# Kernel tuning notes

Hardware: AMD Instinct MI355X
Metric: run time of the kernel (lower is better)

Reference implementation:

```python
import math
import jax, jax.numpy as jnp
import numpy as np

HIDDEN = 1024
N_HEADS = 16
HEAD = HIDDEN // N_HEADS
B = 2
L = 2048
STRIDE = 128
EXPR = 8
MAXPOS = 2048


def _checkpoint(wi):
    if wi % STRIDE == 0 and wi != 0:
        return wi - EXPR
    return (wi // STRIDE) * STRIDE + STRIDE - EXPR


def _subset_summaries(absolute_max):
    ci = _checkpoint(0)
    s = set()
    while ci <= absolute_max - 1:
        s |= set(range(ci, min(ci + EXPR + 1, absolute_max)))
        ci = _checkpoint(ci + STRIDE)
    return s


def build_sparse_mask(n, bidirectional=True):
    # Faithful numpy port of prepare_sparse_mask: -1e4 everywhere, 0 at allowed positions.
    mask = np.full((n, n), -10000.0, dtype=np.float32)
    global_summaries = _subset_summaries(n) if bidirectional else set()
    for i in range(n):
        absolute_max = n if bidirectional else i + 1
        rounded = ((i + STRIDE) // STRIDE) * STRIDE
        if i % STRIDE == 0 and i != 0:
            s1 = set(range(i - STRIDE, min(absolute_max, i + 1)))
        else:
            s1 = set(range(max(0, rounded - STRIDE), min(absolute_max, rounded + 1)))
        s2 = set() if bidirectional else _subset_summaries(absolute_max)
        idx = sorted(s1 | s2 | global_summaries)
        mask[i, idx] = 0.0
    return mask


def setup_inputs() -> dict:
    key = jax.random.key(0)
    ks = jax.random.split(key, 8)
    s = 1.0 / math.sqrt(HIDDEN)
    inp = {
        "hidden_states": jax.random.normal(ks[0], (B, L, HIDDEN), dtype=jnp.float32),
        "attention_mask": jnp.zeros((B, 1, 1, L), dtype=jnp.float32),
        "Wq": jax.random.normal(ks[1], (HIDDEN, HIDDEN), dtype=jnp.float32) * s,
        "bq": jnp.zeros((HIDDEN,), dtype=jnp.float32),
        "Wk": jax.random.normal(ks[2], (HIDDEN, HIDDEN), dtype=jnp.float32) * s,
        "bk": jnp.zeros((HIDDEN,), dtype=jnp.float32),
        "Wv": jax.random.normal(ks[3], (HIDDEN, HIDDEN), dtype=jnp.float32) * s,
        "bv": jnp.zeros((HIDDEN,), dtype=jnp.float32),
        "sparse_mask": jnp.asarray(build_sparse_mask(MAXPOS)[:L, :L]),
    }
    return inp


def _split_heads(x):  # [B, L, H] -> [B, nH, L, hd]
    b, l, _ = x.shape
    return x.reshape(b, l, N_HEADS, HEAD).transpose(0, 2, 1, 3)


def reference(hidden_states, attention_mask, Wq, bq, Wk, bk, Wv, bv, sparse_mask):
    q = _split_heads(hidden_states @ Wq + bq)
    k = _split_heads(hidden_states @ Wk + bk)
    v = _split_heads(hidden_states @ Wv + bv)
    scores = jnp.einsum("bhqd,bhkd->bhqk", q, k) / math.sqrt(HEAD)
    scores = scores + sparse_mask  # [L,L] broadcasts over [B,nH,L,L]
    scores = jnp.clip(scores, -10000.0, 10000.0)
    scores = scores + attention_mask
    probs = jax.nn.softmax(scores.astype(jnp.float32), axis=-1).astype(scores.dtype)
    # dropout prob = 0.0 -> identity
    ctx = jnp.einsum("bhqk,bhkd->bhqd", probs, v)
    return ctx.transpose(0, 2, 1, 3).reshape(hidden_states.shape[0], -1, HIDDEN)
```

## Files before the change

### kernel.cpp

```cpp
#include <hip/hip_runtime.h>

#define HID 1024
#define NH 16
#define HD 64
#define BB 2
#define LL 2048
#define GC 143
#define GP 192

typedef __attribute__((ext_vector_type(8))) __bf16 bf16x8;
typedef __attribute__((ext_vector_type(4))) float f32x4;

__device__ __forceinline__ void gload_lds16(const void* g, void* l) {
  __builtin_amdgcn_global_load_lds((const __attribute__((address_space(1))) void*)g,
                                   (__attribute__((address_space(3))) void*)l, 16, 0, 0);
}

__global__ __launch_bounds__(256) void cvt_hs_kernel(const float* __restrict__ hs,
                                                     __bf16* __restrict__ hsb) {
  int i = blockIdx.x * 256 + threadIdx.x;
  const float4* src = (const float4*)hs;
  float4 a = src[2 * i], b = src[2 * i + 1];
  bf16x8 v;
  v[0] = (__bf16)a.x; v[1] = (__bf16)a.y; v[2] = (__bf16)a.z; v[3] = (__bf16)a.w;
  v[4] = (__bf16)b.x; v[5] = (__bf16)b.y; v[6] = (__bf16)b.z; v[7] = (__bf16)b.w;
  ((bf16x8*)hsb)[i] = v;
}

__global__ __launch_bounds__(256) void cvt_wt_kernel(const float* __restrict__ Wq,
                                                     const float* __restrict__ Wk,
                                                     const float* __restrict__ Wv,
                                                     __bf16* __restrict__ wtb) {
  int kt = blockIdx.x, nt = blockIdx.y, z = blockIdx.z;
  const float* w = (z == 0) ? Wq : (z == 1) ? Wk : Wv;
  __bf16* dst = wtb + (size_t)z * HID * HID;
  __shared__ __bf16 tile[64][66];
  int t = threadIdx.x;
  int cr = t & 63, rr = t >> 6;
#pragma unroll
  for (int it = 0; it < 16; it++) {
    int r = it * 4 + rr;
    tile[cr][r] = (__bf16)w[(size_t)(kt * 64 + r) * HID + nt * 64 + cr];
  }
  __syncthreads();
#pragma unroll
  for (int it = 0; it < 16; it++) {
    int r = it * 4 + rr;
    dst[(size_t)(nt * 64 + r) * HID + kt * 64 + cr] = tile[r][cr];
  }
}

__global__ __launch_bounds__(256) void setup_kernel(const float* __restrict__ amask,
                                                    unsigned int* __restrict__ zbase,
                                                    float* __restrict__ amg) {
  int i = blockIdx.x * 256 + threadIdx.x;
  zbase[i] = 0u;
  if (i < BB * GP) {
    int b = i / GP, cc = i % GP;
    int k = cc / 9, j = cc - 9 * k;
    int col = (cc < GC) ? (120 + 128 * k + j) : 0;
    amg[i] = amask[b * LL + col];
  }
}

__global__ __launch_bounds__(256, 2) void qkv_gemm_kernel(
    const __bf16* __restrict__ hsb, const __bf16* __restrict__ wtb,
    const float* __restrict__ bq, const float* __restrict__ bk,
    const float* __restrict__ bv, __bf16* __restrict__ qb,
    __bf16* __restrict__ kkb, __bf16* __restrict__ vtb,
    __bf16* __restrict__ kgb, __bf16* __restrict__ vgb) {
  int nt = blockIdx.x, mt = blockIdx.y, which = blockIdx.z;
  const __bf16* wt = wtb + (size_t)which * HID * HID;
  const float* bias = (which == 0) ? bq : (which == 1) ? bk : bv;

  __shared__ __bf16 a_lds[128 * 64];
  __shared__ __bf16 b_lds[128 * 64];

  int tid = threadIdx.x;
  int wave = tid >> 6, lane = tid & 63;
  int wm = wave >> 1, wn = wave & 1;
  int lrow = lane & 15, lgr = lane >> 4, g = lane & 7;

  f32x4 acc[4][4];
#pragma unroll
  for (int i = 0; i < 4; i++)
#pragma unroll
    for (int j = 0; j < 4; j++) acc[i][j] = f32x4{0.f, 0.f, 0.f, 0.f};

  for (int kk = 0; kk < HID; kk += 64) {
#pragma unroll
    for (int i = 0; i < 4; i++) {
      int r = (wave * 4 + i) * 8 + (lane >> 3);
      int gs = (g ^ (r & 7)) * 8;
      gload_lds16(hsb + (size_t)(mt * 128 + r) * HID + kk + gs,
                  &a_lds[(wave * 4 + i) * 512]);
      gload_lds16(wt + (size_t)(nt * 128 + r) * HID + kk + gs,
                  &b_lds[(wave * 4 + i) * 512]);
    }
    __syncthreads();
#pragma unroll
    for (int kf = 0; kf < 2; kf++) {
      bf16x8 af[4], bfr[4];
#pragma unroll
      for (int mr = 0; mr < 4; mr++) {
        int row = wm * 64 + mr * 16 + lrow;
        af[mr] = *(const bf16x8*)((const char*)a_lds + row * 128 +
                                  ((kf * 64 + lgr * 16) ^ ((row & 7) << 4)));
      }
#pragma unroll
      for (int nr = 0; nr < 4; nr++) {
        int row = wn * 64 + nr * 16 + lrow;
        bfr[nr] = *(const bf16x8*)((const char*)b_lds + row * 128 +
                                   ((kf * 64 + lgr * 16) ^ ((row & 7) << 4)));
      }
#pragma unroll
      for (int mr = 0; mr < 4; mr++)
#pragma unroll
        for (int nr = 0; nr < 4; nr++)
          acc[mr][nr] = __builtin_amdgcn_mfma_f32_16x16x32_bf16(
              af[mr], bfr[nr], acc[mr][nr], 0, 0, 0);
    }
    __syncthreads();
  }

#pragma unroll
  for (int nr = 0; nr < 4; nr++) {
    int n = nt * 128 + wn * 64 + nr * 16 + lrow;
    float bsv = bias[n];
    int hh = n >> 6, d = n & 63;
#pragma unroll
    for (int mr = 0; mr < 4; mr++) {
#pragma unroll
      for (int reg = 0; reg < 4; reg++) {
        int m = mt * 128 + wm * 64 + mr * 16 + lgr * 4 + reg;
        int bidx = m >> 11, l = m & 2047;
        float val = acc[mr][nr][reg] + bsv;
        int c7 = l & 127;
        bool isg = (c7 >= 120) || (c7 == 0 && l != 0);
        int cidx = (c7 >= 120) ? ((l >> 7) * 9 + (c7 - 120)) : (((l >> 7) - 1) * 9 + 8);
        if (which == 0) {
          val *= 0.125f;
          qb[((size_t)(bidx * NH + hh) * LL + l) * HD + d] = (__bf16)val;
        } else if (which == 1) {
          __bf16 bv16 = (__bf16)val;
          kkb[((size_t)(bidx * NH + hh) * LL + l) * HD + d] = bv16;
          if (isg) kgb[((size_t)(bidx * NH + hh) * GP + cidx) * HD + d] = bv16;
        } else {
          __bf16 bv16 = (__bf16)val;
          vtb[((size_t)(bidx * NH + hh) * HD + d) * LL + l] = bv16;
          if (isg) vgb[((size_t)(bidx * NH + hh) * HD + d) * GP + cidx] = bv16;
        }
      }
    }
  }
}

__global__ __launch_bounds__(256, 2) void attn_kernel(
    const __bf16* __restrict__ qb, const __bf16* __restrict__ kkb,
    const __bf16* __restrict__ vtb, const __bf16* __restrict__ kgb,
    const __bf16* __restrict__ vgb, const float* __restrict__ amg,
    const float* __restrict__ amask, float* __restrict__ out) {
  int qt = blockIdx.x, hh = blockIdx.y, b = blockIdx.z;
  __shared__ __bf16 k_lds[64 * 64];
  __shared__ __bf16 v_lds[64 * 64];
  __shared__ __bf16 p_scr[4][16 * 64];

  int tid = threadIdx.x, wave = tid >> 6, lane = tid & 63;
  int lrow = lane & 15, lgr = lane >> 4, g = lane & 7;

  const __bf16* qbh = qb + (size_t)(b * NH + hh) * LL * HD;
  const __bf16* kbh = kkb + (size_t)(b * NH + hh) * LL * HD;
  const __bf16* vth = vtb + (size_t)(b * NH + hh) * HD * LL;
  const __bf16* kgh = kgb + (size_t)(b * NH + hh) * GP * HD;
  const __bf16* vgh = vgb + (size_t)(b * NH + hh) * HD * GP;

  int qrow = qt * 64 + wave * 16 + lrow;
  bf16x8 qf0 = *(const bf16x8*)(qbh + (size_t)qrow * HD + lgr * 8);
  bf16x8 qf1 = *(const bf16x8*)(qbh + (size_t)qrow * HD + 32 + lgr * 8);

  const float M0 = 20.f;
  float l_part[4];
  f32x4 o_acc[4];
#pragma unroll
  for (int i = 0; i < 4; i++) {
    l_part[i] = 0.f;
    o_acc[i] = f32x4{0.f, 0.f, 0.f, 0.f};
  }
  int myrow = qt * 64 + wave * 16 + lgr * 4;

  bool ext = (qt >= 2) && ((qt & 1) == 0);
  int nlocal = ext ? 4 : 2;
  int lbase = ext ? (qt - 2) : (qt & ~1);
  int ntiles = 3 + nlocal;
  int W = (qt >> 1) * 128;

  for (int it = 0; it < ntiles; it++) {
    bool isglob = (it < 3);
    const __bf16 *ksrc, *vsrc;
    int vstride, colbase;
    if (isglob) {
      colbase = it * 64;
      ksrc = kgh + (size_t)colbase * HD;
      vsrc = vgh + colbase;
      vstride = GP;
    } else {
      colbase = (lbase + (it - 3)) * 64;
      ksrc = kbh + (size_t)colbase * HD;
      vsrc = vth + colbase;
      vstride = LL;
    }
    bool specialonly = ext && (it == 3 || it == 4);
    bool active = !specialonly || (wave == 0);

#pragma unroll
    for (int i = 0; i < 2; i++) {
      int r = (wave * 2 + i) * 8 + (lane >> 3);
      int gs = (g ^ (r & 7)) * 8;
      gload_lds16(ksrc + (size_t)r * HD + gs, &k_lds[(wave * 2 + i) * 512]);
      gload_lds16(vsrc + (size_t)r * vstride + gs, &v_lds[(wave * 2 + i) * 512]);
    }
    __syncthreads();

    if (active) {
      f32x4 s[4];
#pragma unroll
      for (int nr = 0; nr < 4; nr++) {
        int row = nr * 16 + lrow;
        bf16x8 kf0 = *(const bf16x8*)((const char*)k_lds + row * 128 +
                                      ((lgr * 16) ^ ((row & 7) << 4)));
        bf16x8 kf1 = *(const bf16x8*)((const char*)k_lds + row * 128 +
                                      ((64 + lgr * 16) ^ ((row & 7) << 4)));
        f32x4 z = f32x4{0.f, 0.f, 0.f, 0.f};
        z = __builtin_amdgcn_mfma_f32_16x16x32_bf16(qf0, kf0, z, 0, 0, 0);
        z = __builtin_amdgcn_mfma_f32_16x16x32_bf16(qf1, kf1, z, 0, 0, 0);
        s[nr] = z;
      }

#pragma unroll
      for (int nr = 0; nr < 4; nr++) {
        int cc = colbase + nr * 16 + lrow;
        if (isglob) {
          float am = (cc < GC) ? amg[b * GP + cc] : 0.f;
#pragma unroll
          for (int reg = 0; reg < 4; reg++) {
            float v = fminf(fmaxf(s[nr][reg], -10000.f), 10000.f) + am;
            if (cc >= GC) v = -10000.f;
            s[nr][reg] = v;
          }
        } else {
          int c = cc;
          float am = amask[b * LL + c];
          int c7 = c & 127;
          bool gcol = (c7 >= 120) || (c7 == 0 && c != 0);
#pragma unroll
          for (int reg = 0; reg < 4; reg++) {
            int row = myrow + reg;
            bool sp = ((row & 127) == 0) && (row != 0);
            bool allowed = !gcol && (sp ? (c < W) : (c >= W));
            float v = s[nr][reg] + (allowed ? 0.f : -10000.f);
            v = fminf(fmaxf(v, -10000.f), 10000.f) + am;
            s[nr][reg] = v;
          }
        }
      }

#pragma unroll
      for (int reg = 0; reg < 4; reg++) {
#pragma unroll
        for (int nr = 0; nr < 4; nr++) {
          float p = __expf(s[nr][reg] - M0);
          s[nr][reg] = p;
          l_part[reg] += p;
        }
      }

#pragma unroll
      for (int nr = 0; nr < 4; nr++) {
#pragma unroll
        for (int reg = 0; reg < 4; reg++) {
          int rq = lgr * 4 + reg;
          int off = (nr * 32 + lrow * 2) ^ ((rq & 7) << 4);
          *(__bf16*)((char*)&p_scr[wave][0] + rq * 128 + off) = (__bf16)s[nr][reg];
        }
      }
    }
    asm volatile("s_waitcnt lgkmcnt(0)" ::: "memory");
    __builtin_amdgcn_sched_barrier(0);

    if (active) {
      bf16x8 pa0 = *(const bf16x8*)((const char*)&p_scr[wave][0] + lrow * 128 +
                                    ((lgr * 16) ^ ((lrow & 7) << 4)));
      bf16x8 pa1 = *(const bf16x8*)((const char*)&p_scr[wave][0] + lrow * 128 +
                                    ((64 + lgr * 16) ^ ((lrow & 7) << 4)));
#pragma unroll
      for (int nd = 0; nd < 4; nd++) {
        int row = nd * 16 + lrow;
        bf16x8 vf0 = *(const bf16x8*)((const char*)v_lds + row * 128 +
                                      ((lgr * 16) ^ ((row & 7) << 4)));
        bf16x8 vf1 = *(const bf16x8*)((const char*)v_lds + row * 128 +
                                      ((64 + lgr * 16) ^ ((row & 7) << 4)));
        o_acc[nd] = __builtin_amdgcn_mfma_f32_16x16x32_bf16(pa0, vf0, o_acc[nd], 0, 0, 0);
        o_acc[nd] = __builtin_amdgcn_mfma_f32_16x16x32_bf16(pa1, vf1, o_acc[nd], 0, 0, 0);
      }
    }
    __syncthreads();
  }

#pragma unroll
  for (int off = 1; off < 16; off <<= 1)
#pragma unroll
    for (int reg = 0; reg < 4; reg++) l_part[reg] += __shfl_xor(l_part[reg], off);

#pragma unroll
  for (int nd = 0; nd < 4; nd++) {
#pragma unroll
    for (int reg = 0; reg < 4; reg++) {
      int row = myrow + reg;
      int d = nd * 16 + lrow;
      out[((size_t)b * LL + row) * HID + hh * HD + d] =
          o_acc[nd][reg] / l_part[reg];
    }
  }
}

extern "C" void kernel_launch(void* const* d_in, const int* in_sizes, int n_in,
                              void* d_out, int out_size, void* d_ws, size_t ws_size,
                              hipStream_t stream) {
  (void)in_sizes; (void)n_in; (void)out_size; (void)ws_size;
  const float* hs = (const float*)d_in[0];
  const float* amask = (const float*)d_in[1];
  const float* Wq = (const float*)d_in[2];
  const float* bq = (const float*)d_in[3];
  const float* Wk = (const float*)d_in[4];
  const float* bk = (const float*)d_in[5];
  const float* Wv = (const float*)d_in[6];
  const float* bv = (const float*)d_in[7];
  float* out = (float*)d_out;

  char* ws = (char*)d_ws;
  __bf16* hsb = (__bf16*)(ws);
  __bf16* wtb = (__bf16*)(ws + 8388608);
  __bf16* qb  = (__bf16*)(ws + 14680064);
  __bf16* kb  = (__bf16*)(ws + 23068672);
  __bf16* vtb = (__bf16*)(ws + 31457280);
  __bf16* kgb = (__bf16*)(ws + 39845888);
  __bf16* vgb = (__bf16*)(ws + 40632320);
  float*  amg = (float*)(ws + 41418752);

  hipLaunchKernelGGL(cvt_hs_kernel, dim3(2048), dim3(256), 0, stream, hs, hsb);
  hipLaunchKernelGGL(cvt_wt_kernel, dim3(16, 16, 3), dim3(256), 0, stream, Wq, Wk, Wv, wtb);
  hipLaunchKernelGGL(setup_kernel, dim3(1536), dim3(256), 0, stream,
                     amask, (unsigned int*)kgb, amg);
  hipLaunchKernelGGL(qkv_gemm_kernel, dim3(8, 32, 3), dim3(256), 0, stream,
                     hsb, wtb, bq, bk, bv, qb, kb, vtb, kgb, vgb);
  hipLaunchKernelGGL(attn_kernel, dim3(32, 16, 2), dim3(256), 0, stream,
                     qb, kb, vtb, kgb, vgb, amg, amask, out);
}
```

Measured before the change: 80.13 us.

## Realign attention query tiles to sparse windows with double-buffered K/V staging

The attention kernel now uses 512-thread blocks covering 128 query rows, offset by one so that each block lines up with a single local 128-column window. The special checkpoint rows are handled by shifting the windows, with an extra block for row 0 and clamped loads and guarded stores past the end. This drops the per-row sparse-mask logic and the idle-wave tiles, hoists the attention-mask loads out of the loop, and double-buffers the K/V LDS tiles so the next tile loads while the current one is computed. The cost is more LDS per block, a larger block size, and a grid of 17 tiles per head with one partly wasted.

```diff
diff --git a/kernel.cpp b/kernel.cpp
--- a/kernel.cpp
+++ b/kernel.cpp
@@ -155,16 +155,16 @@
   }
 }
 
-__global__ __launch_bounds__(256, 2) void attn_kernel(
+__global__ __launch_bounds__(512, 4) void attn_kernel(
     const __bf16* __restrict__ qb, const __bf16* __restrict__ kkb,
     const __bf16* __restrict__ vtb, const __bf16* __restrict__ kgb,
     const __bf16* __restrict__ vgb, const float* __restrict__ amg,
     const float* __restrict__ amask, float* __restrict__ out) {
+  __shared__ __bf16 kbuf[2][64 * 64];
+  __shared__ __bf16 vbuf[2][64 * 64];
+  __shared__ __bf16 p_scr[8][16 * 64];
+
   int qt = blockIdx.x, hh = blockIdx.y, b = blockIdx.z;
-  __shared__ __bf16 k_lds[64 * 64];
-  __shared__ __bf16 v_lds[64 * 64];
-  __shared__ __bf16 p_scr[4][16 * 64];
-
   int tid = threadIdx.x, wave = tid >> 6, lane = tid & 63;
   int lrow = lane & 15, lgr = lane >> 4, g = lane & 7;
 
@@ -174,9 +174,28 @@
   const __bf16* kgh = kgb + (size_t)(b * NH + hh) * GP * HD;
   const __bf16* vgh = vgb + (size_t)(b * NH + hh) * HD * GP;
 
-  int qrow = qt * 64 + wave * 16 + lrow;
-  bf16x8 qf0 = *(const bf16x8*)(qbh + (size_t)qrow * HD + lgr * 8);
-  bf16x8 qf1 = *(const bf16x8*)(qbh + (size_t)qrow * HD + 32 + lgr * 8);
+  int shift = (qt == 16) ? 0 : 1;
+  int qt2 = (qt == 16) ? 0 : qt;
+  int W = qt2 * 128;
+
+  int qrow = qt2 * 128 + shift + wave * 16 + lrow;
+  int qld = (qrow > LL - 1) ? (LL - 1) : qrow;
+  bf16x8 qf0 = *(const bf16x8*)(qbh + (size_t)qld * HD + lgr * 8);
+  bf16x8 qf1 = *(const bf16x8*)(qbh + (size_t)qld * HD + 32 + lgr * 8);
+
+  float amG[3][4], amL[2][4];
+#pragma unroll
+  for (int it = 0; it < 3; it++)
+#pragma unroll
+    for (int nr = 0; nr < 4; nr++) {
+      int cc = it * 64 + nr * 16 + lrow;
+      amG[it][nr] = (cc < GC) ? amg[b * GP + cc] : 0.f;
+    }
+#pragma unroll
+  for (int it = 0; it < 2; it++)
+#pragma unroll
+    for (int nr = 0; nr < 4; nr++)
+      amL[it][nr] = amask[b * LL + W + it * 64 + nr * 16 + lrow];
 
   const float M0 = 20.f;
   float l_part[4];
@@ -186,125 +205,117 @@
     l_part[i] = 0.f;
     o_acc[i] = f32x4{0.f, 0.f, 0.f, 0.f};
   }
-  int myrow = qt * 64 + wave * 16 + lgr * 4;
-
-  bool ext = (qt >= 2) && ((qt & 1) == 0);
-  int nlocal = ext ? 4 : 2;
-  int lbase = ext ? (qt - 2) : (qt & ~1);
-  int ntiles = 3 + nlocal;
-  int W = (qt >> 1) * 128;
-
-  for (int it = 0; it < ntiles; it++) {
-    bool isglob = (it < 3);
-    const __bf16 *ksrc, *vsrc;
-    int vstride, colbase;
-    if (isglob) {
-      colbase = it * 64;
-      ksrc = kgh + (size_t)colbase * HD;
-      vsrc = vgh + colbase;
-      vstride = GP;
-    } else {
-      colbase = (lbase + (it - 3)) * 64;
-      ksrc = kbh + (size_t)colbase * HD;
-      vsrc = vth + colbase;
-      vstride = LL;
-    }
-    bool specialonly = ext && (it == 3 || it == 4);
-    bool active = !specialonly || (wave == 0);
-
-#pragma unroll
-    for (int i = 0; i < 2; i++) {
-      int r = (wave * 2 + i) * 8 + (lane >> 3);
-      int gs = (g ^ (r & 7)) * 8;
-      gload_lds16(ksrc + (size_t)r * HD + gs, &k_lds[(wave * 2 + i) * 512]);
-      gload_lds16(vsrc + (size_t)r * vstride + gs, &v_lds[(wave * 2 + i) * 512]);
-    }
-    __syncthreads();
-
-    if (active) {
-      f32x4 s[4];
+  int myrow = qt2 * 128 + shift + wave * 16 + lgr * 4;
+
+#define STAGE(IT, BI)                                                     \
+  do {                                                                    \
+    const __bf16 *ks_, *vs_;                                              \
+    int vst_;                                                             \
+    if ((IT) < 3) {                                                       \
+      ks_ = kgh + (size_t)((IT)*64) * HD;                                 \
+      vs_ = vgh + (IT)*64;                                                \
+      vst_ = GP;                                                          \
+    } else {                                                              \
+      int cb_ = W + ((IT)-3) * 64;                                        \
+      ks_ = kbh + (size_t)cb_ * HD;                                       \
+      vs_ = vth + cb_;                                                    \
+      vst_ = LL;                                                          \
+    }                                                                     \
+    int r_ = tid >> 3;                                                    \
+    int gs_ = (g ^ (r_ & 7)) * 8;                                         \
+    gload_lds16(ks_ + (size_t)r_ * HD + gs_, &kbuf[BI][wave * 512]);      \
+    gload_lds16(vs_ + (size_t)r_ * vst_ + gs_, &vbuf[BI][wave * 512]);    \
+  } while (0)
+
+  STAGE(0, 0);
+  __syncthreads();
+
+#pragma unroll
+  for (int it = 0; it < 5; it++) {
+    int cur = it & 1;
+    if (it < 4) STAGE(it + 1, cur ^ 1);
+
+    const __bf16* k_lds = kbuf[cur];
+    const __bf16* v_lds = vbuf[cur];
+    int colbase = (it < 3) ? it * 64 : W + (it - 3) * 64;
+
+    f32x4 s[4];
+#pragma unroll
+    for (int nr = 0; nr < 4; nr++) {
+      int row = nr * 16 + lrow;
+      bf16x8 kf0 = *(const bf16x8*)((const char*)k_lds + row * 128 +
+                                    ((lgr * 16) ^ ((row & 7) << 4)));
+      bf16x8 kf1 = *(const bf16x8*)((const char*)k_lds + row * 128 +
+                                    ((64 + lgr * 16) ^ ((row & 7) << 4)));
+      f32x4 z = f32x4{0.f, 0.f, 0.f, 0.f};
+      z = __builtin_amdgcn_mfma_f32_16x16x32_bf16(qf0, kf0, z, 0, 0, 0);
+      z = __builtin_amdgcn_mfma_f32_16x16x32_bf16(qf1, kf1, z, 0, 0, 0);
+      s[nr] = z;
+    }
+
+#pragma unroll
+    for (int nr = 0; nr < 4; nr++) {
+      if (it < 3) {
+        int cc = colbase + nr * 16 + lrow;
+        float am = amG[it][nr];
+#pragma unroll
+        for (int reg = 0; reg < 4; reg++) {
+          float v = fminf(fmaxf(s[nr][reg], -10000.f), 10000.f) + am;
+          if (cc >= GC) v = -10000.f;
+          s[nr][reg] = v;
+        }
+      } else {
+        int off = (it - 3) * 64 + nr * 16 + lrow;
+        float am = amL[it - 3][nr];
+        bool gcol = (off >= 120) || (off == 0 && W != 0);
+#pragma unroll
+        for (int reg = 0; reg < 4; reg++) {
+          float v = s[nr][reg] + (gcol ? -10000.f : 0.f);
+          v = fminf(fmaxf(v, -10000.f), 10000.f) + am;
+          s[nr][reg] = v;
+        }
+      }
+    }
+
+#pragma unroll
+    for (int reg = 0; reg < 4; reg++) {
 #pragma unroll
       for (int nr = 0; nr < 4; nr++) {
-        int row = nr * 16 + lrow;
-        bf16x8 kf0 = *(const bf16x8*)((const char*)k_lds + row * 128 +
-                                      ((lgr * 16) ^ ((row & 7) << 4)));
-        bf16x8 kf1 = *(const bf16x8*)((const char*)k_lds + row * 128 +
-                                      ((64 + lgr * 16) ^ ((row & 7) << 4)));
-        f32x4 z = f32x4{0.f, 0.f, 0.f, 0.f};
-        z = __builtin_amdgcn_mfma_f32_16x16x32_bf16(qf0, kf0, z, 0, 0, 0);
-        z = __builtin_amdgcn_mfma_f32_16x16x32_bf16(qf1, kf1, z, 0, 0, 0);
-        s[nr] = z;
-      }
-
-#pragma unroll
-      for (int nr = 0; nr < 4; nr++) {
-        int cc = colbase + nr * 16 + lrow;
-        if (isglob) {
-          float am = (cc < GC) ? amg[b * GP + cc] : 0.f;
-#pragma unroll
-          for (int reg = 0; reg < 4; reg++) {
-            float v = fminf(fmaxf(s[nr][reg], -10000.f), 10000.f) + am;
-            if (cc >= GC) v = -10000.f;
-            s[nr][reg] = v;
-          }
-        } else {
-          int c = cc;
-          float am = amask[b * LL + c];
-          int c7 = c & 127;
-          bool gcol = (c7 >= 120) || (c7 == 0 && c != 0);
-#pragma unroll
-          for (int reg = 0; reg < 4; reg++) {
-            int row = myrow + reg;
-            bool sp = ((row & 127) == 0) && (row != 0);
-            bool allowed = !gcol && (sp ? (c < W) : (c >= W));
-            float v = s[nr][reg] + (allowed ? 0.f : -10000.f);
-            v = fminf(fmaxf(v, -10000.f), 10000.f) + am;
-            s[nr][reg] = v;
-          }
-        }
-      }
-
+        float p = __expf(s[nr][reg] - M0);
+        s[nr][reg] = p;
+        l_part[reg] += p;
+      }
+    }
+
+#pragma unroll
+    for (int nr = 0; nr < 4; nr++) {
 #pragma unroll
       for (int reg = 0; reg < 4; reg++) {
-#pragma unroll
-        for (int nr = 0; nr < 4; nr++) {
-          float p = __expf(s[nr][reg] - M0);
-          s[nr][reg] = p;
-          l_part[reg] += p;
-        }
-      }
-
-#pragma unroll
-      for (int nr = 0; nr < 4; nr++) {
-#pragma unroll
-        for (int reg = 0; reg < 4; reg++) {
-          int rq = lgr * 4 + reg;
-          int off = (nr * 32 + lrow * 2) ^ ((rq & 7) << 4);
-          *(__bf16*)((char*)&p_scr[wave][0] + rq * 128 + off) = (__bf16)s[nr][reg];
-        }
+        int rq = lgr * 4 + reg;
+        int off = (nr * 32 + lrow * 2) ^ ((rq & 7) << 4);
+        *(__bf16*)((char*)&p_scr[wave][0] + rq * 128 + off) = (__bf16)s[nr][reg];
       }
     }
     asm volatile("s_waitcnt lgkmcnt(0)" ::: "memory");
     __builtin_amdgcn_sched_barrier(0);
 
-    if (active) {
-      bf16x8 pa0 = *(const bf16x8*)((const char*)&p_scr[wave][0] + lrow * 128 +
-                                    ((lgr * 16) ^ ((lrow & 7) << 4)));
-      bf16x8 pa1 = *(const bf16x8*)((const char*)&p_scr[wave][0] + lrow * 128 +
-                                    ((64 + lgr * 16) ^ ((lrow & 7) << 4)));
-#pragma unroll
-      for (int nd = 0; nd < 4; nd++) {
-        int row = nd * 16 + lrow;
-        bf16x8 vf0 = *(const bf16x8*)((const char*)v_lds + row * 128 +
-                                      ((lgr * 16) ^ ((row & 7) << 4)));
-        bf16x8 vf1 = *(const bf16x8*)((const char*)v_lds + row * 128 +
-                                      ((64 + lgr * 16) ^ ((row & 7) << 4)));
-        o_acc[nd] = __builtin_amdgcn_mfma_f32_16x16x32_bf16(pa0, vf0, o_acc[nd], 0, 0, 0);
-        o_acc[nd] = __builtin_amdgcn_mfma_f32_16x16x32_bf16(pa1, vf1, o_acc[nd], 0, 0, 0);
-      }
+    bf16x8 pa0 = *(const bf16x8*)((const char*)&p_scr[wave][0] + lrow * 128 +
+                                  ((lgr * 16) ^ ((lrow & 7) << 4)));
+    bf16x8 pa1 = *(const bf16x8*)((const char*)&p_scr[wave][0] + lrow * 128 +
+                                  ((64 + lgr * 16) ^ ((lrow & 7) << 4)));
+#pragma unroll
+    for (int nd = 0; nd < 4; nd++) {
+      int row = nd * 16 + lrow;
+      bf16x8 vf0 = *(const bf16x8*)((const char*)v_lds + row * 128 +
+                                    ((lgr * 16) ^ ((row & 7) << 4)));
+      bf16x8 vf1 = *(const bf16x8*)((const char*)v_lds + row * 128 +
+                                    ((64 + lgr * 16) ^ ((row & 7) << 4)));
+      o_acc[nd] = __builtin_amdgcn_mfma_f32_16x16x32_bf16(pa0, vf0, o_acc[nd], 0, 0, 0);
+      o_acc[nd] = __builtin_amdgcn_mfma_f32_16x16x32_bf16(pa1, vf1, o_acc[nd], 0, 0, 0);
     }
     __syncthreads();
   }
+#undef STAGE
 
 #pragma unroll
   for (int off = 1; off < 16; off <<= 1)
@@ -316,9 +327,11 @@
 #pragma unroll
     for (int reg = 0; reg < 4; reg++) {
       int row = myrow + reg;
-      int d = nd * 16 + lrow;
-      out[((size_t)b * LL + row) * HID + hh * HD + d] =
-          o_acc[nd][reg] / l_part[reg];
+      if (row < LL) {
+        int d = nd * 16 + lrow;
+        out[((size_t)b * LL + row) * HID + hh * HD + d] =
+            o_acc[nd][reg] / l_part[reg];
+      }
     }
   }
 }
@@ -353,6 +366,6 @@
                      amask, (unsigned int*)kgb, amg);
   hipLaunchKernelGGL(qkv_gemm_kernel, dim3(8, 32, 3), dim3(256), 0, stream,
                      hsb, wtb, bq, bk, bv, qb, kb, vtb, kgb, vgb);
-  hipLaunchKernelGGL(attn_kernel, dim3(32, 16, 2), dim3(256), 0, stream,
+  hipLaunchKernelGGL(attn_kernel, dim3(17, NH, BB), dim3(512), 0, stream,
                      qb, kb, vtb, kgb, vgb, amg, amask, out);
 }
```

Result: faster. 75.23 us (-6.1%).
